# Optimization experiments

Hardware: AMD Instinct MI355X
Metric: run time of the kernel (lower is better)

Reference implementation:

```python
import jax, jax.numpy as jnp
import numpy as np

L = 28       # spectral bands
M = 256      # rows
N = 256      # cols (== patch_size, so phi crop is identity)
STRIDE = 2   # dispersion shift per band


def setup_inputs() -> dict:
    key = jax.random.key(0)
    kx, kp = jax.random.split(key)
    x = jax.random.normal(kx, (32, L, M, N), dtype=jnp.float32)
    # binary coded aperture: (1 + sign(randn)) / 2, repeated over bands
    phi2d = (1.0 + jnp.sign(jax.random.normal(kp, (M, N), dtype=jnp.float32))) / 2.0
    phi = jnp.broadcast_to(phi2d[None, :, :], (L, M, N)).astype(jnp.float32)
    return {"x": x, "phi": phi}


def reference(x, phi):
    """CASSI forward: A^T(A(x)) with coded-aperture mask phi.

    x:   [B, L, M, N] hyperspectral cube
    phi: [L, M, N]    coded aperture (binary mask)
    returns [B, L, M, N]
    """
    B = x.shape[0]
    n_out = N + STRIDE * (L - 1)  # dispersed measurement width (310)

    # --- get_measurement: mask then per-band shift-and-sum ---
    y1 = x * phi[None]  # einsum('blmn,lmn->blmn')
    # column index each (band l, col n) lands on after dispersion
    idx = (jnp.arange(N)[None, :] + STRIDE * jnp.arange(L)[:, None]).reshape(-1)  # [L*N]
    vals = jnp.transpose(y1, (0, 2, 1, 3)).reshape(B, M, L * N)  # [B, M, L*N]
    # fused shift-scatter-add instead of L pad+accumulate passes
    y2 = jnp.zeros((B, M, n_out), dtype=x.dtype).at[:, :, idx].add(vals)  # [B, M, 310]

    # --- get_transpose: gather shifted windows, re-mask ---
    xt = y2[:, :, idx].reshape(B, M, L, N)          # [B, M, L, N]
    xt = jnp.transpose(xt, (0, 2, 1, 3))            # [B, L, M, N]
    return xt * phi[None]
```

## Files before the change

kernel.cpp:

```cpp
#include <hip/hip_runtime.h>


constexpr int L_BANDS = 28;
constexpr int M_DIM   = 256;
constexpr int N_DIM   = 256;
constexpr int SHIFT   = 2;
constexpr int N_OUT   = N_DIM + SHIFT * (L_BANDS - 1);
constexpr int MN      = M_DIM * N_DIM;

__global__ __launch_bounds__(320) void cassi_fwd_kernel(
    const float* __restrict__ x,
    const float* __restrict__ phi,
    float* __restrict__ out)
{
    const int c = threadIdx.x;
    if (c >= N_OUT) return;

    const int bm = blockIdx.x;
    const int b  = bm >> 8;
    const int m  = bm & (M_DIM - 1);

    const float* xb = x   + b * (L_BANDS * MN) + m * N_DIM;
    const float* pb = phi +                      m * N_DIM;
    float*       ob = out + b * (L_BANDS * MN) + m * N_DIM;

    float xr[L_BANDS];
    float pr[L_BANDS];

    #pragma unroll
    for (int l = 0; l < L_BANDS; ++l) {
        const int n = c - SHIFT * l;
        const bool v = (unsigned)n < (unsigned)N_DIM;
        xr[l] = v ? xb[l * MN + n] : 0.0f;
        pr[l] = v ? pb[l * MN + n] : 0.0f;
    }

    float acc = 0.0f;
    #pragma unroll
    for (int l = 0; l < L_BANDS; ++l) {
        acc += xr[l] * pr[l];
    }

    #pragma unroll
    for (int l = 0; l < L_BANDS; ++l) {
        const int n = c - SHIFT * l;
        if ((unsigned)n < (unsigned)N_DIM) {
            ob[l * MN + n] = pr[l] * acc;
        }
    }
}

extern "C" void kernel_launch(void* const* d_in, const int* in_sizes, int n_in,
                              void* d_out, int out_size, void* d_ws, size_t ws_size,
                              hipStream_t stream) {
    const float* x   = (const float*)d_in[0];
    const float* phi = (const float*)d_in[1];
    float*       out = (float*)d_out;

    const int B = in_sizes[0] / (L_BANDS * MN);

    dim3 grid(B * M_DIM);
    dim3 block(320);
    cassi_fwd_kernel<<<grid, block, 0, stream>>>(x, phi, out);
}
```

Baseline: 100.3 us.

## Process column pairs with float2 loads/stores, two rows per block, nontemporal stores

Each thread now handles two adjacent output columns using 8-byte vector loads and stores, and each 320-thread block covers two rows instead of one. Because the dispersion shift is even, a pair is either fully valid or fully invalid, which keeps the boundary logic simple. Output is written with nontemporal stores so the large output stream does not pollute the cache. The aim is fewer memory instructions and better utilisation of threads per block, at the cost of more registers per thread.

```diff
diff --git a/kernel.cpp b/kernel.cpp
--- a/kernel.cpp
+++ b/kernel.cpp
@@ -6,36 +6,46 @@
 constexpr int N_DIM   = 256;
 constexpr int SHIFT   = 2;
 constexpr int N_OUT   = N_DIM + SHIFT * (L_BANDS - 1);
+constexpr int NPAIR   = N_OUT / 2;
 constexpr int MN      = M_DIM * N_DIM;
+
+typedef float v2f __attribute__((ext_vector_type(2)));
 
 __global__ __launch_bounds__(320) void cassi_fwd_kernel(
     const float* __restrict__ x,
     const float* __restrict__ phi,
     float* __restrict__ out)
 {
-    const int c = threadIdx.x;
-    if (c >= N_OUT) return;
+    const int t = threadIdx.x;
+    const int r = (t >= 160) ? 1 : 0;
+    const int p = t - 160 * r;
+    if (p >= NPAIR) return;
 
-    const int bm = blockIdx.x;
-    const int b  = bm >> 8;
-    const int m  = bm & (M_DIM - 1);
+    const int b  = blockIdx.x >> 7;
+    const int m  = ((blockIdx.x & 127) << 1) + r;
+    const int c0 = p << 1;
 
     const float* xb = x   + b * (L_BANDS * MN) + m * N_DIM;
     const float* pb = phi +                      m * N_DIM;
     float*       ob = out + b * (L_BANDS * MN) + m * N_DIM;
 
-    float xr[L_BANDS];
-    float pr[L_BANDS];
+    v2f xr[L_BANDS];
+    v2f pr[L_BANDS];
 
     #pragma unroll
     for (int l = 0; l < L_BANDS; ++l) {
-        const int n = c - SHIFT * l;
-        const bool v = (unsigned)n < (unsigned)N_DIM;
-        xr[l] = v ? xb[l * MN + n] : 0.0f;
-        pr[l] = v ? pb[l * MN + n] : 0.0f;
+        const int n0 = c0 - SHIFT * l;
+        const bool v = (unsigned)n0 < (unsigned)(N_DIM - 1);
+        if (v) {
+            xr[l] = *(const v2f*)(xb + l * MN + n0);
+            pr[l] = *(const v2f*)(pb + l * MN + n0);
+        } else {
+            xr[l] = (v2f)(0.0f);
+            pr[l] = (v2f)(0.0f);
+        }
     }
 
-    float acc = 0.0f;
+    v2f acc = (v2f)(0.0f);
     #pragma unroll
     for (int l = 0; l < L_BANDS; ++l) {
         acc += xr[l] * pr[l];
@@ -43,9 +53,10 @@
 
     #pragma unroll
     for (int l = 0; l < L_BANDS; ++l) {
-        const int n = c - SHIFT * l;
-        if ((unsigned)n < (unsigned)N_DIM) {
-            ob[l * MN + n] = pr[l] * acc;
+        const int n0 = c0 - SHIFT * l;
+        if ((unsigned)n0 < (unsigned)(N_DIM - 1)) {
+            v2f o = pr[l] * acc;
+            __builtin_nontemporal_store(o, (v2f*)(ob + l * MN + n0));
         }
     }
 }
@@ -59,7 +70,7 @@
 
     const int B = in_sizes[0] / (L_BANDS * MN);
 
-    dim3 grid(B * M_DIM);
+    dim3 grid(B * (M_DIM / 2));
     dim3 block(320);
     cassi_fwd_kernel<<<grid, block, 0, stream>>>(x, phi, out);
 }
```

Result: faster. 80.99 us (-19.3%).
